# Performance work log

Measured on AMD Instinct MI355X. Metric: run time of the kernel, lower is better.

## Reference

```python
import jax, jax.numpy as jnp
import numpy as np

V, E, H2, T = 50000, 256, 512, 16  # vocab, embed, hidden_dim, tagset
H = H2 // 2                        # per-direction hidden
START, STOP = 14, 15
NEG = -10000.0


def setup_inputs() -> dict:
    key = jax.random.key(0)
    ks = jax.random.split(key, 13)
    s = 0.08
    tokens = jax.random.randint(ks[0], (32, 512), 0, V)
    embed_table = jax.random.normal(ks[1], (V, E), jnp.float32)
    Wi_f = jax.random.normal(ks[2], (4 * H, E), jnp.float32) * s
    Wh_f = jax.random.normal(ks[3], (4 * H, H), jnp.float32) * s
    bi_f = jnp.zeros((4 * H,), jnp.float32)
    bh_f = jnp.zeros((4 * H,), jnp.float32)
    Wi_b = jax.random.normal(ks[4], (4 * H, E), jnp.float32) * s
    Wh_b = jax.random.normal(ks[5], (4 * H, H), jnp.float32) * s
    bi_b = jnp.zeros((4 * H,), jnp.float32)
    bh_b = jnp.zeros((4 * H,), jnp.float32)
    Wt = jax.random.normal(ks[6], (T, H2), jnp.float32) * s
    bt = jnp.zeros((T,), jnp.float32)
    trans = jax.random.normal(ks[7], (T, T), jnp.float32)
    trans = trans.at[START, :].set(NEG).at[:, STOP].set(NEG)
    return {"tokens": tokens, "embed_table": embed_table,
            "Wi_f": Wi_f, "Wh_f": Wh_f, "bi_f": bi_f, "bh_f": bh_f,
            "Wi_b": Wi_b, "Wh_b": Wh_b, "bi_b": bi_b, "bh_b": bh_b,
            "Wt": Wt, "bt": bt, "transitions": trans}


def _lstm_dir(x, Wi, Wh, bi, bh, reverse=False):
    # x: [S, B, E] -> h seq [S, B, H], PyTorch gate order i,f,g,o
    S, B, _ = x.shape
    xs = x[::-1] if reverse else x
    pre = jnp.einsum('sbe,ge->sbg', xs, Wi) + bi + bh  # precompute input GEMM

    def step(carry, z_t):
        h, c = carry
        z = z_t + h @ Wh.T  # [B, 4H]
        i, f, g, o = jnp.split(z, 4, axis=-1)
        c = jax.nn.sigmoid(f) * c + jax.nn.sigmoid(i) * jnp.tanh(g)
        h = jax.nn.sigmoid(o) * jnp.tanh(c)
        return (h, c), h

    h0 = jnp.zeros((B, H), x.dtype)
    _, hs = jax.lax.scan(step, (h0, h0), pre)
    return hs[::-1] if reverse else hs


def reference(tokens, embed_table, Wi_f, Wh_f, bi_f, bh_f,
              Wi_b, Wh_b, bi_b, bh_b, Wt, bt, transitions):
    x = embed_table[tokens]                # [B, S, E]
    x = jnp.transpose(x, (1, 0, 2))        # [S, B, E] seq-first like nn.LSTM
    hf = _lstm_dir(x, Wi_f, Wh_f, bi_f, bh_f, reverse=False)
    hb = _lstm_dir(x, Wi_b, Wh_b, bi_b, bh_b, reverse=True)
    feats = jnp.concatenate([hf, hb], axis=-1)           # [S, B, 2H]
    emissions = jnp.einsum('sbh,th->sbt', feats, Wt) + bt  # [S, B, T]

    B = tokens.shape[0]
    alpha0 = jnp.full((B, T), NEG, jnp.float32).at[:, START].set(0.0)

    def crf_step(alpha, emit_t):
        # alpha: [B, T_prev]; transitions[next, prev]; emit_t: [B, T_next]
        scores = alpha[:, None, :] + transitions[None, :, :] + emit_t[:, :, None]
        return jax.nn.logsumexp(scores, axis=2), None

    alpha, _ = jax.lax.scan(crf_step, alpha0, emissions)
    log_Z = jax.nn.logsumexp(alpha + transitions[STOP][None, :], axis=1)  # [B]
    return log_Z
```

## Files before the change

### kernel.cpp

```cpp
#include <hip/hip_runtime.h>
#include <hip/hip_bf16.h>
#include <stdint.h>

#define NSLICE 4

typedef __attribute__((ext_vector_type(4))) float f32x4;
typedef __attribute__((ext_vector_type(8))) short bf16x8;

#define WS_XBF   0u
#define WS_WIR   8388608u
#define WS_BIAS  9437184u
#define WS_PRE   9445376u
#define WS_HALL  76554240u
#define WS_FLAGS 93364224u
#define WS_EMIS  93368320u
#define WS_CHK   94416896u

__device__ __forceinline__ unsigned short f2bf(float x) {
    union { float f; unsigned int u; } v; v.f = x;
    return (unsigned short)((v.u + 0x7FFFu + ((v.u >> 16) & 1u)) >> 16);
}
__device__ __forceinline__ float bf2f(unsigned short b) {
    union { float f; unsigned int u; } v; v.u = ((unsigned int)b) << 16; return v.f;
}
__device__ __forceinline__ unsigned int pack2(float a, float b) {
    return (unsigned int)f2bf(a) | ((unsigned int)f2bf(b) << 16);
}
__device__ __forceinline__ float sigf(float x)  { return 1.0f / (1.0f + __expf(-x)); }
__device__ __forceinline__ float tanhf_(float x){ return 1.0f - 2.0f / (__expf(2.0f * x) + 1.0f); }

__global__ __launch_bounds__(256) void k_prep(
    const int* __restrict__ tokens, const float* __restrict__ embed,
    const float* __restrict__ Wi_f, const float* __restrict__ Wi_b,
    const float* __restrict__ bi_f, const float* __restrict__ bh_f,
    const float* __restrict__ bi_b, const float* __restrict__ bh_b,
    char* __restrict__ ws)
{
    int blk = blockIdx.x, tid = threadIdx.x;
    unsigned short* xbf  = (unsigned short*)(ws + WS_XBF);
    unsigned short* wir  = (unsigned short*)(ws + WS_WIR);
    float* biasr         = (float*)(ws + WS_BIAS);
    if (blk < 2048) {
        int rr = tid >> 5, cc = tid & 31;
        int r = blk * 8 + rr;
        int s = r >> 5, b = r & 31;
        int tok = tokens[b * 512 + s];
        int k = cc * 8;
        const float* src = embed + (size_t)tok * 256 + k;
        float4 a = *(const float4*)src;
        float4 c = *(const float4*)(src + 4);
        uint4 o; o.x = pack2(a.x, a.y); o.y = pack2(a.z, a.w);
        o.z = pack2(c.x, c.y); o.w = pack2(c.z, c.w);
        *(uint4*)(xbf + (size_t)r * 256 + k) = o;
    } else if (blk < 2304) {
        int rr = tid >> 5, cc = tid & 31;
        int rowp = (blk - 2048) * 8 + rr;
        int dir = rowp >> 10, q = rowp & 1023;
        int j = q >> 8, rs = q & 255;
        int g = rs >> 6, hl = rs & 63;
        int srow = g * 256 + j * 64 + hl;
        const float* W = dir ? Wi_b : Wi_f;
        int k = cc * 8;
        const float* src = W + (size_t)srow * 256 + k;
        float4 a = *(const float4*)src;
        float4 c = *(const float4*)(src + 4);
        uint4 o; o.x = pack2(a.x, a.y); o.y = pack2(a.z, a.w);
        o.z = pack2(c.x, c.y); o.w = pack2(c.z, c.w);
        *(uint4*)(wir + (size_t)rowp * 256 + k) = o;
        if (cc == 0)
            biasr[rowp] = dir ? (bi_b[srow] + bh_b[srow]) : (bi_f[srow] + bh_f[srow]);
    } else {
        int g = (blk - 2304) * 256 + tid;
        for (int u = g; u < 9216; u += 4096) {
            if (u < 1024) ((int*)(ws + WS_FLAGS))[u] = 0;
            else if (u < 5120) ((unsigned int*)(ws + WS_HALL))[u - 1024] = 0;
            else ((unsigned int*)(ws + WS_HALL + (size_t)513 * 16384))[u - 5120] = 0;
        }
    }
}

__global__ __launch_bounds__(256) void k_pregemm(char* __restrict__ ws)
{
    __shared__ unsigned short Asb[128 * 136];
    __shared__ unsigned short Bsb[64 * 136];
    const unsigned short* xbf = (const unsigned short*)(ws + WS_XBF);
    const unsigned short* wir = (const unsigned short*)(ws + WS_WIR);
    const float* biasr        = (const float*)(ws + WS_BIAS);
    unsigned short* pre       = (unsigned short*)(ws + WS_PRE);
    int blk = blockIdx.x, tid = threadIdx.x;
    int mb = blk >> 5, nb = blk & 31;
    int Mbase = mb * 128, Nbase = nb * 64;
    int w = tid >> 6, l = tid & 63, col = l & 15, quad = l >> 4;
    f32x4 acc[4][2];
    #pragma unroll
    for (int a = 0; a < 4; ++a)
        #pragma unroll
        for (int b = 0; b < 2; ++b) acc[a][b] = (f32x4){0.f, 0.f, 0.f, 0.f};

    for (int kh = 0; kh < 2; ++kh) {
        __syncthreads();
        #pragma unroll
        for (int i = 0; i < 8; ++i) {
            int c = tid + i * 256;
            int row = c >> 4, c16 = c & 15;
            uint4 v = *(const uint4*)(xbf + ((size_t)(Mbase + row) * 256 + kh * 128 + c16 * 8));
            *(uint4*)(Asb + row * 136 + c16 * 8) = v;
        }
        #pragma unroll
        for (int i = 0; i < 4; ++i) {
            int c = tid + i * 256;
            int row = c >> 4, c16 = c & 15;
            uint4 v = *(const uint4*)(wir + ((size_t)(Nbase + row) * 256 + kh * 128 + c16 * 8));
            *(uint4*)(Bsb + row * 136 + c16 * 8) = v;
        }
        __syncthreads();
        int mhalf = w >> 1, nh = w & 1;
        #pragma unroll
        for (int kt = 0; kt < 4; ++kt) {
            bf16x8 bfr[2];
            #pragma unroll
            for (int nn = 0; nn < 2; ++nn)
                bfr[nn] = *(const bf16x8*)(Bsb + (16 * (nh * 2 + nn) + col) * 136 + kt * 32 + quad * 8);
            #pragma unroll
            for (int mm = 0; mm < 4; ++mm) {
                bf16x8 afr = *(const bf16x8*)(Asb + (16 * (mhalf * 4 + mm) + col) * 136 + kt * 32 + quad * 8);
                #pragma unroll
                for (int nn = 0; nn < 2; ++nn)
                    acc[mm][nn] = __builtin_amdgcn_mfma_f32_16x16x32_bf16(afr, bfr[nn], acc[mm][nn], 0, 0, 0);
            }
        }
    }
    #pragma unroll
    for (int mm = 0; mm < 4; ++mm) {
        int m_t = (w >> 1) * 4 + mm;
        int s = (Mbase >> 5) + (m_t >> 1);
        int bhalf = m_t & 1;
        #pragma unroll
        for (int nn = 0; nn < 2; ++nn) {
            int ncol = Nbase + 16 * ((w & 1) * 2 + nn) + col;
            int dir = ncol >> 10, j = (ncol >> 8) & 3, r = ncol & 255;
            int g = r >> 6, hl16 = (r >> 4) & 3;
            int tidp = (bhalf * 4 + hl16) * 64 + l;
            float bv = biasr[ncol];
            f32x4 a = acc[mm][nn];
            uint2 o;
            o.x = pack2(a[0] + bv, a[1] + bv);
            o.y = pack2(a[2] + bv, a[3] + bv);
            size_t off = (((size_t)(dir * 512 + s) * 4 + j) * 512 + tidp) * 16 + g * 4;
            *(uint2*)(pre + off) = o;
        }
    }
}

__global__ __launch_bounds__(512, 2) void k_rec(
    const float* __restrict__ Wh_f, const float* __restrict__ Wh_b, char* __restrict__ ws)
{
    __shared__ unsigned short hbuf[32 * 264];
    __shared__ unsigned short hst[8 * 16 * 20];
    int blk = blockIdx.x, tid = threadIdx.x;
    int dir = blk >> 2, j = blk & 3;
    int w = tid >> 6, l = tid & 63, col = l & 15, quad = l >> 4;
    int m = w >> 2, hl16 = w & 3;
    const float* Wh = dir ? Wh_b : Wh_f;
    const unsigned short* pre = (const unsigned short*)(ws + WS_PRE);
    unsigned short* hall      = (unsigned short*)(ws + WS_HALL);
    int* flags                = (int*)(ws + WS_FLAGS);

    bf16x8 wf[4][8];
    #pragma unroll
    for (int g = 0; g < 4; ++g) {
        int grow = g * 256 + j * 64 + hl16 * 16 + col;
        #pragma unroll
        for (int kt = 0; kt < 8; ++kt) {
            const float* src = Wh + (size_t)grow * 256 + kt * 32 + quad * 8;
            float4 x0 = *(const float4*)src;
            float4 x1 = *(const float4*)(src + 4);
            bf16x8 f;
            f[0] = (short)f2bf(x0.x); f[1] = (short)f2bf(x0.y);
            f[2] = (short)f2bf(x0.z); f[3] = (short)f2bf(x0.w);
            f[4] = (short)f2bf(x1.x); f[5] = (short)f2bf(x1.y);
            f[6] = (short)f2bf(x1.z); f[7] = (short)f2bf(x1.w);
            wf[g][kt] = f;
        }
    }
    float cst[4] = {0.f, 0.f, 0.f, 0.f};
    size_t hbase_u = (size_t)dir * 513 * 8192;

    for (int st = 0; st < 512; ++st) {
        int s = dir ? (511 - st) : st;
        const uint4* pp = (const uint4*)(pre + ((((size_t)(dir * 512 + s)) * 4 + j) * 512 + tid) * 16);
        uint4 p0 = pp[0], p1 = pp[1];
        if (st > 0 && tid == 0) {
            while (__hip_atomic_load(flags + (dir * 512 + st - 1),
                                     __ATOMIC_ACQUIRE, __HIP_MEMORY_SCOPE_AGENT) < NSLICE) {}
        }
        __syncthreads();
        {
            const uint4* hsrc = (const uint4*)(hall + hbase_u + (size_t)st * 8192);
            #pragma unroll
            for (int i = 0; i < 2; ++i) {
                int c = tid + i * 512;
                int row = c >> 5, c16 = c & 31;
                uint4 v = hsrc[row * 32 + c16];
                *(uint4*)(hbuf + row * 264 + c16 * 8) = v;
            }
        }
        __syncthreads();
        f32x4 acc[4];
        #pragma unroll
        for (int g = 0; g < 4; ++g) acc[g] = (f32x4){0.f, 0.f, 0.f, 0.f};
        #pragma unroll
        for (int kt = 0; kt < 8; ++kt) {
            bf16x8 af = *(const bf16x8*)(hbuf + (m * 16 + col) * 264 + kt * 32 + quad * 8);
            #pragma unroll
            for (int g = 0; g < 4; ++g)
                acc[g] = __builtin_amdgcn_mfma_f32_16x16x32_bf16(af, wf[g][kt], acc[g], 0, 0, 0);
        }
        unsigned int pw[8] = {p0.x, p0.y, p0.z, p0.w, p1.x, p1.y, p1.z, p1.w};
        float z[4][4];
        #pragma unroll
        for (int g = 0; g < 4; ++g) {
            #pragma unroll
            for (int r2 = 0; r2 < 2; ++r2) {
                unsigned int u = pw[g * 2 + r2];
                z[g][r2 * 2]     = acc[g][r2 * 2]     + bf2f((unsigned short)(u & 0xffff));
                z[g][r2 * 2 + 1] = acc[g][r2 * 2 + 1] + bf2f((unsigned short)(u >> 16));
            }
        }
        unsigned short hb16[4];
        #pragma unroll
        for (int r = 0; r < 4; ++r) {
            float ci = sigf(z[1][r]) * cst[r] + sigf(z[0][r]) * tanhf_(z[2][r]);
            cst[r] = ci;
            hb16[r] = f2bf(sigf(z[3][r]) * tanhf_(ci));
        }
        unsigned short* hw = hst + w * 320;
        #pragma unroll
        for (int r = 0; r < 4; ++r) hw[(quad * 4 + r) * 20 + col] = hb16[r];
        int rrow = l >> 2, cpart = l & 3;
        uint2 hv = *(const uint2*)(hw + rrow * 20 + cpart * 4);
        size_t dsto = hbase_u + (size_t)(st + 1) * 8192 + (size_t)(m * 16 + rrow) * 256
                    + j * 64 + hl16 * 16 + cpart * 4;
        *(uint2*)(hall + dsto) = hv;
        __syncthreads();
        if (tid == 0)
            __hip_atomic_fetch_add(flags + (dir * 512 + st), 1,
                                   __ATOMIC_RELEASE, __HIP_MEMORY_SCOPE_AGENT);
    }
}

__global__ __launch_bounds__(256) void k_emis(
    const float* __restrict__ Wt, const float* __restrict__ bt, char* __restrict__ ws)
{
    __shared__ float WtL[16 * 528];
    __shared__ unsigned short hrow[16 * 536];
    __shared__ float btL[16];
    int blk = blockIdx.x, tid = threadIdx.x;
    int sbb = blk * 16;
    int s = sbb >> 5, bbase = sbb & 31;
    const unsigned short* hall = (const unsigned short*)(ws + WS_HALL);
    float* emis = (float*)(ws + WS_EMIS);
    #pragma unroll
    for (int i = 0; i < 8; ++i) {
        int c = tid + i * 256;
        int trow = c >> 7, c128 = c & 127;
        float4 v = *(const float4*)(Wt + (size_t)trow * 512 + c128 * 4);
        *(float4*)(WtL + trow * 528 + c128 * 4) = v;
    }
    #pragma unroll
    for (int i = 0; i < 4; ++i) {
        int c = tid + i * 256;
        int row = c >> 6, c6 = c & 63, half = c6 >> 5, c16 = c6 & 31;
        size_t base = half == 0 ? (size_t)(s + 1) * 8192 : ((size_t)513 + (512 - s)) * 8192;
        uint4 v = *(const uint4*)(hall + base + (size_t)(bbase + row) * 256 + c16 * 8);
        *(uint4*)(hrow + row * 536 + half * 256 + c16 * 8) = v;
    }
    if (tid < 16) btL[tid] = bt[tid];
    __syncthreads();
    int t = tid >> 4, i = tid & 15;
    float acc = btL[t];
    const float* wrow = WtL + t * 528;
    const unsigned short* hr = hrow + i * 536;
    #pragma unroll 8
    for (int k = 0; k < 512; k += 4) {
        uint2 hu = *(const uint2*)(hr + k);
        float4 wv = *(const float4*)(wrow + k);
        acc += bf2f((unsigned short)(hu.x & 0xffff)) * wv.x
             + bf2f((unsigned short)(hu.x >> 16))    * wv.y
             + bf2f((unsigned short)(hu.y & 0xffff)) * wv.z
             + bf2f((unsigned short)(hu.y >> 16))    * wv.w;
    }
    emis[((size_t)(bbase + i) * 512 + s) * 16 + t] = acc;
}

__global__ __launch_bounds__(256) void k_crfc(const float* __restrict__ trans, char* __restrict__ ws)
{
    __shared__ float trL[16 * 17];
    __shared__ float est[16 * 16];
    __shared__ float Pb[2][16 * 17];
    int blk = blockIdx.x, tid = threadIdx.x;
    int b = blk >> 5, c = blk & 31;
    int t = tid >> 4, p = tid & 15;
    const float* emis = (const float*)(ws + WS_EMIS);
    float* chk = (float*)(ws + WS_CHK);
    trL[t * 17 + p] = trans[t * 16 + p];
    est[t * 16 + p] = emis[((size_t)b * 512 + c * 16 + t) * 16 + p];
    __syncthreads();
    float tr[16];
    #pragma unroll
    for (int q = 0; q < 16; ++q) tr[q] = trL[t * 17 + q];
    float out = trL[t * 17 + p] + est[0 * 16 + t];
    Pb[0][t * 17 + p] = out;
    __syncthreads();
    int cur = 0;
    for (int si = 1; si < 16; ++si) {
        float v[16]; float mx = -3.0e38f;
        #pragma unroll
        for (int q = 0; q < 16; ++q) { v[q] = tr[q] + Pb[cur][q * 17 + p]; mx = fmaxf(mx, v[q]); }
        float ss = 0.f;
        #pragma unroll
        for (int q = 0; q < 16; ++q) ss += __expf(v[q] - mx);
        out = est[si * 16 + t] + mx + __logf(ss);
        Pb[1 - cur][t * 17 + p] = out;
        __syncthreads();
        cur = 1 - cur;
    }
    chk[(size_t)(b * 32 + c) * 256 + t * 16 + p] = out;
}

__global__ __launch_bounds__(256) void k_crff(
    const float* __restrict__ trans, char* __restrict__ ws, float* __restrict__ out)
{
    __shared__ float Cst[16 * 17];
    __shared__ float Pb[2][16 * 17];
    __shared__ float af[16];
    int b = blockIdx.x, tid = threadIdx.x;
    int t = tid >> 4, p = tid & 15;
    const float* chk = (const float*)(ws + WS_CHK);
    Pb[0][t * 17 + p] = chk[(size_t)(b * 32) * 256 + t * 16 + p];
    __syncthreads();
    int cur = 0;
    for (int ci = 1; ci < 32; ++ci) {
        Cst[t * 17 + p] = chk[(size_t)(b * 32 + ci) * 256 + t * 16 + p];
        __syncthreads();
        float v[16]; float mx = -3.0e38f;
        #pragma unroll
        for (int q = 0; q < 16; ++q) { v[q] = Cst[t * 17 + q] + Pb[cur][q * 17 + p]; mx = fmaxf(mx, v[q]); }
        float ss = 0.f;
        #pragma unroll
        for (int q = 0; q < 16; ++q) ss += __expf(v[q] - mx);
        float outv = mx + __logf(ss);
        Pb[1 - cur][t * 17 + p] = outv;
        __syncthreads();
        cur = 1 - cur;
    }
    float vfin = Pb[cur][t * 17 + p] + ((p == 14) ? 0.0f : -10000.0f);
    Cst[t * 17 + p] = vfin;
    __syncthreads();
    if (tid < 16) {
        float mx = -3.0e38f;
        for (int q = 0; q < 16; ++q) mx = fmaxf(mx, Cst[tid * 17 + q]);
        float ss = 0.f;
        for (int q = 0; q < 16; ++q) ss += __expf(Cst[tid * 17 + q] - mx);
        af[tid] = mx + __logf(ss) + trans[15 * 16 + tid];
    }
    __syncthreads();
    if (tid == 0) {
        float mx = -3.0e38f;
        for (int q = 0; q < 16; ++q) mx = fmaxf(mx, af[q]);
        float ss = 0.f;
        for (int q = 0; q < 16; ++q) ss += __expf(af[q] - mx);
        out[b] = mx + __logf(ss);
    }
}

extern "C" void kernel_launch(void* const* d_in, const int* in_sizes, int n_in,
                              void* d_out, int out_size, void* d_ws, size_t ws_size,
                              hipStream_t stream)
{
    const int*   tokens = (const int*)d_in[0];
    const float* embed  = (const float*)d_in[1];
    const float* Wi_f   = (const float*)d_in[2];
    const float* Wh_f   = (const float*)d_in[3];
    const float* bi_f   = (const float*)d_in[4];
    const float* bh_f   = (const float*)d_in[5];
    const float* Wi_b   = (const float*)d_in[6];
    const float* Wh_b   = (const float*)d_in[7];
    const float* bi_b   = (const float*)d_in[8];
    const float* bh_b   = (const float*)d_in[9];
    const float* Wt     = (const float*)d_in[10];
    const float* bt     = (const float*)d_in[11];
    const float* trans  = (const float*)d_in[12];
    char* ws = (char*)d_ws;
    float* out = (float*)d_out;

    hipLaunchKernelGGL(k_prep, dim3(2320), dim3(256), 0, stream,
                       tokens, embed, Wi_f, Wi_b, bi_f, bh_f, bi_b, bh_b, ws);
    hipLaunchKernelGGL(k_pregemm, dim3(4096), dim3(256), 0, stream, ws);
    hipLaunchKernelGGL(k_rec, dim3(8), dim3(512), 0, stream, Wh_f, Wh_b, ws);
    hipLaunchKernelGGL(k_emis, dim3(1024), dim3(256), 0, stream, Wt, bt, ws);
    hipLaunchKernelGGL(k_crfc, dim3(1024), dim3(256), 0, stream, trans, ws);
    hipLaunchKernelGGL(k_crff, dim3(32), dim3(256), 0, stream, trans, ws, out);
}
```

Measured before the change: 1.827 ms.

## Replace flag-counter barrier with sentinel-valued data polling in recurrent kernel

The recurrent LSTM kernel no longer uses a per-step atomic counter and a single-thread spin followed by block barriers. k_prep now fills every hidden-state slot except slot 0 with an all-ones sentinel. Each thread polls its own 8-byte chunks of the previous h with atomic loads until the sentinel is gone, and reads its own slice from shared memory. This removes a barrier plus the flag round-trip on each step, at the cost of many more atomic polls to memory and a larger init pass that writes the whole hidden buffer. It also assumes an all-ones bit pattern can never be a valid bf16 h value.

```diff
diff --git a/kernel.cpp b/kernel.cpp
--- a/kernel.cpp
+++ b/kernel.cpp
@@ -2,17 +2,16 @@
 #include <hip/hip_bf16.h>
 #include <stdint.h>
 
-#define NSLICE 4
-
 typedef __attribute__((ext_vector_type(4))) float f32x4;
 typedef __attribute__((ext_vector_type(8))) short bf16x8;
+
+#define SENT 0xFFFFFFFFFFFFFFFFULL
 
 #define WS_XBF   0u
 #define WS_WIR   8388608u
 #define WS_BIAS  9437184u
 #define WS_PRE   9445376u
 #define WS_HALL  76554240u
-#define WS_FLAGS 93364224u
 #define WS_EMIS  93368320u
 #define WS_CHK   94416896u
 
@@ -70,11 +69,15 @@
         if (cc == 0)
             biasr[rowp] = dir ? (bi_b[srow] + bh_b[srow]) : (bi_f[srow] + bh_f[srow]);
     } else {
-        int g = (blk - 2304) * 256 + tid;
-        for (int u = g; u < 9216; u += 4096) {
-            if (u < 1024) ((int*)(ws + WS_FLAGS))[u] = 0;
-            else if (u < 5120) ((unsigned int*)(ws + WS_HALL))[u - 1024] = 0;
-            else ((unsigned int*)(ws + WS_HALL + (size_t)513 * 16384))[u - 5120] = 0;
+        size_t g = (size_t)(blk - 2304) * 256 + tid;
+        uint4* hall4 = (uint4*)(ws + WS_HALL);
+        const unsigned int NF = 0xFFFFFFFFu;
+        for (size_t u = g; u < 1050624u; u += 65536u) {
+            size_t slot = (u >> 10) % 513u;
+            uint4 val;
+            if (slot == 0) { val.x = 0u; val.y = 0u; val.z = 0u; val.w = 0u; }
+            else           { val.x = NF; val.y = NF; val.z = NF; val.w = NF; }
+            hall4[u] = val;
         }
     }
 }
@@ -164,7 +167,6 @@
     const float* Wh = dir ? Wh_b : Wh_f;
     const unsigned short* pre = (const unsigned short*)(ws + WS_PRE);
     unsigned short* hall      = (unsigned short*)(ws + WS_HALL);
-    int* flags                = (int*)(ws + WS_FLAGS);
 
     bf16x8 wf[4][8];
     #pragma unroll
@@ -183,6 +185,9 @@
             wf[g][kt] = f;
         }
     }
+    for (int u = tid; u < 1280; u += 512) ((unsigned int*)hst)[u] = 0;
+    __syncthreads();
+
     float cst[4] = {0.f, 0.f, 0.f, 0.f};
     size_t hbase_u = (size_t)dir * 513 * 8192;
 
@@ -190,22 +195,39 @@
         int s = dir ? (511 - st) : st;
         const uint4* pp = (const uint4*)(pre + ((((size_t)(dir * 512 + s)) * 4 + j) * 512 + tid) * 16);
         uint4 p0 = pp[0], p1 = pp[1];
-        if (st > 0 && tid == 0) {
-            while (__hip_atomic_load(flags + (dir * 512 + st - 1),
-                                     __ATOMIC_ACQUIRE, __HIP_MEMORY_SCOPE_AGENT) < NSLICE) {}
-        }
-        __syncthreads();
-        {
-            const uint4* hsrc = (const uint4*)(hall + hbase_u + (size_t)st * 8192);
-            #pragma unroll
-            for (int i = 0; i < 2; ++i) {
-                int c = tid + i * 512;
-                int row = c >> 5, c16 = c & 31;
-                uint4 v = hsrc[row * 32 + c16];
-                *(uint4*)(hbuf + row * 264 + c16 * 8) = v;
+
+        unsigned short* hsl = hall + hbase_u + (size_t)st * 8192;
+        unsigned long long v[4];
+        int rows[4], c8s[4];
+        bool own[4];
+        #pragma unroll
+        for (int i = 0; i < 4; ++i) {
+            int q = tid + i * 512;
+            int row = q >> 6, c8 = q & 63;
+            rows[i] = row; c8s[i] = c8;
+            own[i] = (c8 >= j * 16) && (c8 < j * 16 + 16);
+            if (!own[i])
+                v[i] = __hip_atomic_fetch_add((unsigned long long*)(hsl + (size_t)q * 4), 0ULL,
+                                              __ATOMIC_RELAXED, __HIP_MEMORY_SCOPE_AGENT);
+        }
+        #pragma unroll
+        for (int i = 0; i < 4; ++i) {
+            if (own[i]) {
+                int lc = c8s[i] * 4 - j * 64;
+                int hl = lc >> 4, c4 = lc & 15;
+                int wp = (rows[i] >> 4) * 4 + hl, r_in = rows[i] & 15;
+                v[i] = *(const unsigned long long*)(hst + wp * 320 + r_in * 20 + c4);
+            } else {
+                while (v[i] == SENT)
+                    v[i] = __hip_atomic_fetch_add((unsigned long long*)(hsl + (size_t)(tid + i * 512) * 4),
+                                                  0ULL, __ATOMIC_RELAXED, __HIP_MEMORY_SCOPE_AGENT);
             }
         }
-        __syncthreads();
+        #pragma unroll
+        for (int i = 0; i < 4; ++i)
+            *(unsigned long long*)(hbuf + rows[i] * 264 + c8s[i] * 4) = v[i];
+        __syncthreads();
+
         f32x4 acc[4];
         #pragma unroll
         for (int g = 0; g < 4; ++g) acc[g] = (f32x4){0.f, 0.f, 0.f, 0.f};
@@ -238,14 +260,12 @@
         #pragma unroll
         for (int r = 0; r < 4; ++r) hw[(quad * 4 + r) * 20 + col] = hb16[r];
         int rrow = l >> 2, cpart = l & 3;
-        uint2 hv = *(const uint2*)(hw + rrow * 20 + cpart * 4);
+        unsigned long long hv = *(const unsigned long long*)(hw + rrow * 20 + cpart * 4);
         size_t dsto = hbase_u + (size_t)(st + 1) * 8192 + (size_t)(m * 16 + rrow) * 256
                     + j * 64 + hl16 * 16 + cpart * 4;
-        *(uint2*)(hall + dsto) = hv;
-        __syncthreads();
-        if (tid == 0)
-            __hip_atomic_fetch_add(flags + (dir * 512 + st), 1,
-                                   __ATOMIC_RELEASE, __HIP_MEMORY_SCOPE_AGENT);
+        (void)__hip_atomic_exchange((unsigned long long*)(hall + dsto), hv,
+                                    __ATOMIC_RELAXED, __HIP_MEMORY_SCOPE_AGENT);
+        __syncthreads();
     }
 }
 
@@ -394,7 +414,7 @@
     char* ws = (char*)d_ws;
     float* out = (float*)d_out;
 
-    hipLaunchKernelGGL(k_prep, dim3(2320), dim3(256), 0, stream,
+    hipLaunchKernelGGL(k_prep, dim3(2560), dim3(256), 0, stream,
                        tokens, embed, Wi_f, Wi_b, bi_f, bh_f, bi_b, bh_b, ws);
     hipLaunchKernelGGL(k_pregemm, dim3(4096), dim3(256), 0, stream, ws);
     hipLaunchKernelGGL(k_rec, dim3(8), dim3(512), 0, stream, Wh_f, Wh_b, ws);
```

New measurement: 1.611 ms. 1.13x faster.

## Split LSTM recurrence by batch halves to drop cross-block flag sync

Applied to the files above, without the earlier changes.

The recurrent kernel changes from 8 blocks that split the hidden dimension (4 slices per direction, synchronised every step through global atomic flags) to 4 blocks. Each block owns half the batch and the full hidden state, so per-step spin-waits on global flags go away. The hidden state now stays in a double-buffered LDS array instead of being re-read from global memory each step. Three gate weight sets stay in registers, while the output-gate weights are pre-packed to bf16 in the prep kernel and streamed from global memory each step, which adds memory traffic and doubles the MFMA work per wave. The pre-activation layout is changed to match the new thread mapping, and the zeroing of the flag and hidden-state buffers is removed.

```diff
diff --git a/kernel.cpp b/kernel.cpp
--- a/kernel.cpp
+++ b/kernel.cpp
@@ -1,8 +1,6 @@
 #include <hip/hip_runtime.h>
 #include <hip/hip_bf16.h>
 #include <stdint.h>
-
-#define NSLICE 4
 
 typedef __attribute__((ext_vector_type(4))) float f32x4;
 typedef __attribute__((ext_vector_type(8))) short bf16x8;
@@ -12,9 +10,9 @@
 #define WS_BIAS  9437184u
 #define WS_PRE   9445376u
 #define WS_HALL  76554240u
-#define WS_FLAGS 93364224u
 #define WS_EMIS  93368320u
 #define WS_CHK   94416896u
+#define WS_OP    93368320u
 
 __device__ __forceinline__ unsigned short f2bf(float x) {
     union { float f; unsigned int u; } v; v.f = x;
@@ -22,6 +20,9 @@
 }
 __device__ __forceinline__ float bf2f(unsigned short b) {
     union { float f; unsigned int u; } v; v.u = ((unsigned int)b) << 16; return v.f;
+}
+__device__ __forceinline__ float bfh(unsigned int w, int hi) {
+    return bf2f((unsigned short)(hi ? (w >> 16) : (w & 0xffff)));
 }
 __device__ __forceinline__ unsigned int pack2(float a, float b) {
     return (unsigned int)f2bf(a) | ((unsigned int)f2bf(b) << 16);
@@ -34,6 +35,7 @@
     const float* __restrict__ Wi_f, const float* __restrict__ Wi_b,
     const float* __restrict__ bi_f, const float* __restrict__ bh_f,
     const float* __restrict__ bi_b, const float* __restrict__ bh_b,
+    const float* __restrict__ Wh_f, const float* __restrict__ Wh_b,
     char* __restrict__ ws)
 {
     int blk = blockIdx.x, tid = threadIdx.x;
@@ -55,10 +57,7 @@
     } else if (blk < 2304) {
         int rr = tid >> 5, cc = tid & 31;
         int rowp = (blk - 2048) * 8 + rr;
-        int dir = rowp >> 10, q = rowp & 1023;
-        int j = q >> 8, rs = q & 255;
-        int g = rs >> 6, hl = rs & 63;
-        int srow = g * 256 + j * 64 + hl;
+        int dir = rowp >> 10, srow = rowp & 1023;
         const float* W = dir ? Wi_b : Wi_f;
         int k = cc * 8;
         const float* src = W + (size_t)srow * 256 + k;
@@ -70,11 +69,17 @@
         if (cc == 0)
             biasr[rowp] = dir ? (bi_b[srow] + bh_b[srow]) : (bi_f[srow] + bh_f[srow]);
     } else {
-        int g = (blk - 2304) * 256 + tid;
-        for (int u = g; u < 9216; u += 4096) {
-            if (u < 1024) ((int*)(ws + WS_FLAGS))[u] = 0;
-            else if (u < 5120) ((unsigned int*)(ws + WS_HALL))[u - 1024] = 0;
-            else ((unsigned int*)(ws + WS_HALL + (size_t)513 * 16384))[u - 5120] = 0;
+        unsigned short* opk = (unsigned short*)(ws + WS_OP);
+        int base = (blk - 2304) * 256 + tid;
+        #pragma unroll
+        for (int i = 0; i < 16; ++i) {
+            int u = base * 16 + i;
+            int j = u & 7, lq = (u >> 3) & 63, kt = (u >> 9) & 7;
+            int hg = (u >> 12) & 1, wv = (u >> 13) & 7, dr = (u >> 16) & 1;
+            int colp = lq & 15, quadp = lq >> 4;
+            const float* W = dr ? Wh_b : Wh_f;
+            float x = W[(size_t)(768 + wv * 32 + hg * 16 + colp) * 256 + kt * 32 + quadp * 8 + j];
+            opk[u] = f2bf(x);
         }
     }
 }
@@ -134,19 +139,19 @@
     for (int mm = 0; mm < 4; ++mm) {
         int m_t = (w >> 1) * 4 + mm;
         int s = (Mbase >> 5) + (m_t >> 1);
-        int bhalf = m_t & 1;
+        int bh = m_t & 1;
         #pragma unroll
         for (int nn = 0; nn < 2; ++nn) {
             int ncol = Nbase + 16 * ((w & 1) * 2 + nn) + col;
-            int dir = ncol >> 10, j = (ncol >> 8) & 3, r = ncol & 255;
-            int g = r >> 6, hl16 = (r >> 4) & 3;
-            int tidp = (bhalf * 4 + hl16) * 64 + l;
+            int dir = ncol >> 10, q = ncol & 1023;
+            int g = q >> 8, hid = q & 255;
+            int wr = hid >> 5, hg = (hid >> 4) & 1;
             float bv = biasr[ncol];
             f32x4 a = acc[mm][nn];
             uint2 o;
             o.x = pack2(a[0] + bv, a[1] + bv);
             o.y = pack2(a[2] + bv, a[3] + bv);
-            size_t off = (((size_t)(dir * 512 + s) * 4 + j) * 512 + tidp) * 16 + g * 4;
+            size_t off = (((((size_t)dir * 512 + s) * 2 + bh) * 8 + wr) * 64 + l) * 32 + hg * 16 + g * 4;
             *(uint2*)(pre + off) = o;
         }
     }
@@ -155,97 +160,80 @@
 __global__ __launch_bounds__(512, 2) void k_rec(
     const float* __restrict__ Wh_f, const float* __restrict__ Wh_b, char* __restrict__ ws)
 {
-    __shared__ unsigned short hbuf[32 * 264];
-    __shared__ unsigned short hst[8 * 16 * 20];
-    int blk = blockIdx.x, tid = threadIdx.x;
-    int dir = blk >> 2, j = blk & 3;
+    __shared__ unsigned short hb[2][16 * 264];
+    int blk = blockIdx.x, tid = threadIdx.x;
+    int dir = blk >> 1, bh = blk & 1;
     int w = tid >> 6, l = tid & 63, col = l & 15, quad = l >> 4;
-    int m = w >> 2, hl16 = w & 3;
     const float* Wh = dir ? Wh_b : Wh_f;
     const unsigned short* pre = (const unsigned short*)(ws + WS_PRE);
+    const unsigned short* opk = (const unsigned short*)(ws + WS_OP);
     unsigned short* hall      = (unsigned short*)(ws + WS_HALL);
-    int* flags                = (int*)(ws + WS_FLAGS);
-
-    bf16x8 wf[4][8];
-    #pragma unroll
-    for (int g = 0; g < 4; ++g) {
-        int grow = g * 256 + j * 64 + hl16 * 16 + col;
-        #pragma unroll
-        for (int kt = 0; kt < 8; ++kt) {
-            const float* src = Wh + (size_t)grow * 256 + kt * 32 + quad * 8;
-            float4 x0 = *(const float4*)src;
-            float4 x1 = *(const float4*)(src + 4);
-            bf16x8 f;
-            f[0] = (short)f2bf(x0.x); f[1] = (short)f2bf(x0.y);
-            f[2] = (short)f2bf(x0.z); f[3] = (short)f2bf(x0.w);
-            f[4] = (short)f2bf(x1.x); f[5] = (short)f2bf(x1.y);
-            f[6] = (short)f2bf(x1.z); f[7] = (short)f2bf(x1.w);
-            wf[g][kt] = f;
-        }
-    }
-    float cst[4] = {0.f, 0.f, 0.f, 0.f};
-    size_t hbase_u = (size_t)dir * 513 * 8192;
+
+    bf16x8 wf[3][2][8];
+    #pragma unroll
+    for (int g = 0; g < 3; ++g)
+        #pragma unroll
+        for (int hg = 0; hg < 2; ++hg) {
+            int nrow = g * 256 + w * 32 + hg * 16 + col;
+            #pragma unroll
+            for (int kt = 0; kt < 8; ++kt) {
+                const float* src = Wh + (size_t)nrow * 256 + kt * 32 + quad * 8;
+                float4 x0 = *(const float4*)src;
+                float4 x1 = *(const float4*)(src + 4);
+                bf16x8 f;
+                f[0] = (short)f2bf(x0.x); f[1] = (short)f2bf(x0.y);
+                f[2] = (short)f2bf(x0.z); f[3] = (short)f2bf(x0.w);
+                f[4] = (short)f2bf(x1.x); f[5] = (short)f2bf(x1.y);
+                f[6] = (short)f2bf(x1.z); f[7] = (short)f2bf(x1.w);
+                wf[g][hg][kt] = f;
+            }
+        }
+    for (int u = tid; u < 2112; u += 512) ((unsigned int*)hb[0])[u] = 0;
+    __syncthreads();
+
+    float cst[8] = {0.f, 0.f, 0.f, 0.f, 0.f, 0.f, 0.f, 0.f};
+    size_t hallbase = (size_t)dir * 513 * 8192;
 
     for (int st = 0; st < 512; ++st) {
         int s = dir ? (511 - st) : st;
-        const uint4* pp = (const uint4*)(pre + ((((size_t)(dir * 512 + s)) * 4 + j) * 512 + tid) * 16);
-        uint4 p0 = pp[0], p1 = pp[1];
-        if (st > 0 && tid == 0) {
-            while (__hip_atomic_load(flags + (dir * 512 + st - 1),
-                                     __ATOMIC_ACQUIRE, __HIP_MEMORY_SCOPE_AGENT) < NSLICE) {}
-        }
-        __syncthreads();
-        {
-            const uint4* hsrc = (const uint4*)(hall + hbase_u + (size_t)st * 8192);
-            #pragma unroll
-            for (int i = 0; i < 2; ++i) {
-                int c = tid + i * 512;
-                int row = c >> 5, c16 = c & 31;
-                uint4 v = hsrc[row * 32 + c16];
-                *(uint4*)(hbuf + row * 264 + c16 * 8) = v;
+        const unsigned short* prl = pre + (((((size_t)dir * 512 + s) * 2 + bh) * 8 + w) * 64 + l) * 32;
+        const unsigned short* cur = hb[st & 1];
+        unsigned short* nxt = hb[(st + 1) & 1];
+        size_t gb = hallbase + (size_t)(st + 1) * 8192 + (size_t)(bh * 16) * 256 + w * 32 + col;
+
+        #pragma unroll
+        for (int hg = 0; hg < 2; ++hg) {
+            f32x4 acc[4];
+            #pragma unroll
+            for (int g = 0; g < 4; ++g) acc[g] = (f32x4){0.f, 0.f, 0.f, 0.f};
+            #pragma unroll
+            for (int kt = 0; kt < 8; ++kt) {
+                bf16x8 af = *(const bf16x8*)(cur + col * 264 + kt * 32 + quad * 8);
+                bf16x8 of = *(const bf16x8*)(opk + ((((size_t)dir * 8 + w) * 2 + hg) * 8 + kt) * 512
+                                                   + (size_t)l * 8);
+                acc[0] = __builtin_amdgcn_mfma_f32_16x16x32_bf16(af, wf[0][hg][kt], acc[0], 0, 0, 0);
+                acc[1] = __builtin_amdgcn_mfma_f32_16x16x32_bf16(af, wf[1][hg][kt], acc[1], 0, 0, 0);
+                acc[2] = __builtin_amdgcn_mfma_f32_16x16x32_bf16(af, wf[2][hg][kt], acc[2], 0, 0, 0);
+                acc[3] = __builtin_amdgcn_mfma_f32_16x16x32_bf16(af, of,            acc[3], 0, 0, 0);
             }
-        }
-        __syncthreads();
-        f32x4 acc[4];
-        #pragma unroll
-        for (int g = 0; g < 4; ++g) acc[g] = (f32x4){0.f, 0.f, 0.f, 0.f};
-        #pragma unroll
-        for (int kt = 0; kt < 8; ++kt) {
-            bf16x8 af = *(const bf16x8*)(hbuf + (m * 16 + col) * 264 + kt * 32 + quad * 8);
-            #pragma unroll
-            for (int g = 0; g < 4; ++g)
-                acc[g] = __builtin_amdgcn_mfma_f32_16x16x32_bf16(af, wf[g][kt], acc[g], 0, 0, 0);
-        }
-        unsigned int pw[8] = {p0.x, p0.y, p0.z, p0.w, p1.x, p1.y, p1.z, p1.w};
-        float z[4][4];
-        #pragma unroll
-        for (int g = 0; g < 4; ++g) {
-            #pragma unroll
-            for (int r2 = 0; r2 < 2; ++r2) {
-                unsigned int u = pw[g * 2 + r2];
-                z[g][r2 * 2]     = acc[g][r2 * 2]     + bf2f((unsigned short)(u & 0xffff));
-                z[g][r2 * 2 + 1] = acc[g][r2 * 2 + 1] + bf2f((unsigned short)(u >> 16));
+            uint4 pa = *(const uint4*)(prl + hg * 16);
+            uint4 pb = *(const uint4*)(prl + hg * 16 + 8);
+            unsigned int pw[8] = {pa.x, pa.y, pa.z, pa.w, pb.x, pb.y, pb.z, pb.w};
+            #pragma unroll
+            for (int r = 0; r < 4; ++r) {
+                float zi = acc[0][r] + bfh(pw[0 + (r >> 1)], r & 1);
+                float zf = acc[1][r] + bfh(pw[2 + (r >> 1)], r & 1);
+                float zg = acc[2][r] + bfh(pw[4 + (r >> 1)], r & 1);
+                float zo = acc[3][r] + bfh(pw[6 + (r >> 1)], r & 1);
+                int ci = hg * 4 + r;
+                float c_ = sigf(zf) * cst[ci] + sigf(zi) * tanhf_(zg);
+                cst[ci] = c_;
+                unsigned short hv = f2bf(sigf(zo) * tanhf_(c_));
+                nxt[(quad * 4 + r) * 264 + w * 32 + hg * 16 + col] = hv;
+                hall[gb + (size_t)(quad * 4 + r) * 256 + hg * 16] = hv;
             }
         }
-        unsigned short hb16[4];
-        #pragma unroll
-        for (int r = 0; r < 4; ++r) {
-            float ci = sigf(z[1][r]) * cst[r] + sigf(z[0][r]) * tanhf_(z[2][r]);
-            cst[r] = ci;
-            hb16[r] = f2bf(sigf(z[3][r]) * tanhf_(ci));
-        }
-        unsigned short* hw = hst + w * 320;
-        #pragma unroll
-        for (int r = 0; r < 4; ++r) hw[(quad * 4 + r) * 20 + col] = hb16[r];
-        int rrow = l >> 2, cpart = l & 3;
-        uint2 hv = *(const uint2*)(hw + rrow * 20 + cpart * 4);
-        size_t dsto = hbase_u + (size_t)(st + 1) * 8192 + (size_t)(m * 16 + rrow) * 256
-                    + j * 64 + hl16 * 16 + cpart * 4;
-        *(uint2*)(hall + dsto) = hv;
-        __syncthreads();
-        if (tid == 0)
-            __hip_atomic_fetch_add(flags + (dir * 512 + st), 1,
-                                   __ATOMIC_RELEASE, __HIP_MEMORY_SCOPE_AGENT);
+        __syncthreads();
     }
 }
 
@@ -394,10 +382,10 @@
     char* ws = (char*)d_ws;
     float* out = (float*)d_out;
 
-    hipLaunchKernelGGL(k_prep, dim3(2320), dim3(256), 0, stream,
-                       tokens, embed, Wi_f, Wi_b, bi_f, bh_f, bi_b, bh_b, ws);
+    hipLaunchKernelGGL(k_prep, dim3(2336), dim3(256), 0, stream,
+                       tokens, embed, Wi_f, Wi_b, bi_f, bh_f, bi_b, bh_b, Wh_f, Wh_b, ws);
     hipLaunchKernelGGL(k_pregemm, dim3(4096), dim3(256), 0, stream, ws);
-    hipLaunchKernelGGL(k_rec, dim3(8), dim3(512), 0, stream, Wh_f, Wh_b, ws);
+    hipLaunchKernelGGL(k_rec, dim3(4), dim3(512), 0, stream, Wh_f, Wh_b, ws);
     hipLaunchKernelGGL(k_emis, dim3(1024), dim3(256), 0, stream, Wt, bt, ws);
     hipLaunchKernelGGL(k_crfc, dim3(1024), dim3(256), 0, stream, trans, ws);
     hipLaunchKernelGGL(k_crff, dim3(32), dim3(256), 0, stream, trans, ws, out);
```

Result: slower. 2.786 ms (+52.5%).
